# Kernel tuning notes

Measured on AMD Instinct MI355X. Metric: run time of the kernel, lower is better.

## Reference

```python
import jax, jax.numpy as jnp
import numpy as np

DIM = 256; K = 3; PAD = 1; DIL = 1; B = 16; H = 56; W = 56
SP = 8           # share_planes
RADIX = 2
ATTN = max(DIM * RADIX // 4, 32)   # 128
EMB = K * K * DIM // SP            # 288

def conv(x, w, pad=0, dil=1, groups=1):
    return jax.lax.conv_general_dilated(
        x, w, (1, 1), [(pad, pad), (pad, pad)], rhs_dilation=(dil, dil),
        feature_group_count=groups, dimension_numbers=('NCHW', 'OIHW', 'NCHW'))

def bn(x, g, b, m, v, eps=1e-5):
    # eval-mode BatchNorm2d
    s = g * jax.lax.rsqrt(v + eps)
    return x * s[None, :, None, None] + (b - m * s)[None, :, None, None]

def gn(x, g, b, groups, eps=1e-5):
    Bb, C, Hh, Ww = x.shape
    xg = x.reshape(Bb, groups, C // groups, Hh, Ww)
    mu = xg.mean((2, 3, 4), keepdims=True)
    var = xg.var((2, 3, 4), keepdims=True)
    xg = (xg - mu) * jax.lax.rsqrt(var + eps)
    return xg.reshape(Bb, C, Hh, Ww) * g[None, :, None, None] + b[None, :, None, None]

def unfold3(x):
    # im2col for 3x3, stride 1, pad 1 -> (B, C, K*K, H, W)
    Bb, C, Hh, Ww = x.shape
    p = (K - 1) // 2
    xp = jnp.pad(x, ((0, 0), (0, 0), (p, p), (p, p)))
    return jnp.stack([xp[:, :, i:i + Hh, j:j + Ww] for i in range(K) for j in range(K)], axis=2)

def reference(x, ke_w, ke_g, ke_b, ke_m, ke_v, e1_w, e1_g, e1_b, e1_m, e1_v,
              e2_w, e2_b, gng, gnb, c1_w, c1_g, c1_b, c1_m, c1_v,
              b2_g, b2_b, b2_m, b2_v, s1_w, s1_b, s1_g, s1_bb, s1_m, s1_v,
              s2_w, s2_b):
    Bb = x.shape[0]
    # key embed: grouped kxk conv + BN + ReLU
    k = jax.nn.relu(bn(conv(x, ke_w, pad=PAD, dil=DIL, groups=4), ke_g, ke_b, ke_m, ke_v))
    qk = jnp.concatenate([x, k], axis=1)                     # (B, 2*DIM, H, W)
    # dynamic kernel branch
    wemb = jax.nn.relu(bn(conv(qk, e1_w), e1_g, e1_b, e1_m, e1_v))
    wemb = conv(wemb, e2_w) + e2_b[None, :, None, None]
    wemb = gn(wemb, gng, gnb, DIM // SP)                     # GroupNorm(dim//8 groups)
    wemb = wemb.reshape(Bb, DIM // SP, K * K, H, W)
    # value branch
    xq = bn(conv(x, c1_w), c1_g, c1_b, c1_m, c1_v)
    # local dynamic convolution: per-pixel kernel shared across SP channels
    patches = unfold3(xq).reshape(Bb, DIM // SP, SP, K * K, H, W)
    y = (patches * wemb[:, :, None]).sum(3).reshape(Bb, DIM, H, W)
    y = bn(y, b2_g, b2_b, b2_m, b2_v)
    y = y * jax.nn.sigmoid(y)                                # swish
    # split attention over radix=2 branches (y, k)
    xs = jnp.stack([y, k], axis=2)                           # (B, C, 2, H, W)
    gap = xs.sum(2).mean((2, 3), keepdims=True)              # (B, C, 1, 1)
    a = jax.nn.relu(bn(conv(gap, s1_w) + s1_b[None, :, None, None], s1_g, s1_bb, s1_m, s1_v))
    a = conv(a, s2_w) + s2_b[None, :, None, None]            # (B, 2*C, 1, 1)
    a = jax.nn.softmax(a.reshape(Bb, DIM, RADIX), axis=2)
    out = (xs * a[:, :, :, None, None]).sum(2)
    return out

def setup_inputs():
    key = jax.random.key(0)
    ks = iter(jax.random.split(key, 40))
    def n(shape, s=1.0):
        return jax.random.normal(next(ks), shape, jnp.float32) * s
    def u(shape):
        return jax.random.uniform(next(ks), shape, jnp.float32, minval=0.5, maxval=1.5)
    d = {}
    d['x'] = n((B, DIM, H, W))
    d['ke_w'] = n((DIM, DIM // 4, K, K), 0.05)
    d['ke_g'] = u((DIM,)); d['ke_b'] = n((DIM,), 0.1); d['ke_m'] = n((DIM,), 0.1); d['ke_v'] = u((DIM,))
    d['e1_w'] = n((DIM // 2, 2 * DIM, 1, 1), 0.05)
    d['e1_g'] = u((DIM // 2,)); d['e1_b'] = n((DIM // 2,), 0.1); d['e1_m'] = n((DIM // 2,), 0.1); d['e1_v'] = u((DIM // 2,))
    d['e2_w'] = n((EMB, DIM // 2, 1, 1), 0.05); d['e2_b'] = n((EMB,), 0.1)
    d['gng'] = u((EMB,)); d['gnb'] = n((EMB,), 0.1)
    d['c1_w'] = n((DIM, DIM, 1, 1), 0.05)
    d['c1_g'] = u((DIM,)); d['c1_b'] = n((DIM,), 0.1); d['c1_m'] = n((DIM,), 0.1); d['c1_v'] = u((DIM,))
    d['b2_g'] = u((DIM,)); d['b2_b'] = n((DIM,), 0.1); d['b2_m'] = n((DIM,), 0.1); d['b2_v'] = u((DIM,))
    d['s1_w'] = n((ATTN, DIM, 1, 1), 0.05); d['s1_b'] = n((ATTN,), 0.1)
    d['s1_g'] = u((ATTN,)); d['s1_bb'] = n((ATTN,), 0.1); d['s1_m'] = n((ATTN,), 0.1); d['s1_v'] = u((ATTN,))
    d['s2_w'] = n((RADIX * DIM, ATTN, 1, 1), 0.05); d['s2_b'] = n((RADIX * DIM,), 0.1)
    return d
```

## Files before the change

### kernel.cpp

```cpp
#include <hip/hip_runtime.h>
#include <hip/hip_bf16.h>

typedef __hip_bfloat16 bf16;
typedef float f32x4 __attribute__((ext_vector_type(4)));
typedef short s16x8 __attribute__((ext_vector_type(8)));

#define NPIX 3136
#define HDIM 56
#define CDIM 256
#define PPIX 3364

static __device__ __forceinline__ float b2f(bf16 v){ return __bfloat162float(v); }
static __device__ __forceinline__ bf16  f2b(float v){ return __float2bfloat16(v); }

#define O_KE_S 0
#define O_KE_B 256
#define O_E1_S 512
#define O_E1_B 640
#define O_C1_S 768
#define O_C1_B 1024
#define O_B2_S 1280
#define O_B2_B 1536
#define O_S1_S 1792
#define O_S1_B 1920
#define O_E2B  2048
#define O_GNS  2336
#define O_GAP  3360
#define O_ATT  7456

__global__ void prep(
    const float* __restrict__ kew, const float* __restrict__ e1w,
    const float* __restrict__ e2w, const float* __restrict__ c1w,
    const float* keg, const float* keb, const float* kem, const float* kev,
    const float* e1g, const float* e1b, const float* e1m, const float* e1v,
    const float* e2b,
    const float* c1g, const float* c1b, const float* c1m, const float* c1v,
    const float* b2g, const float* b2b, const float* b2m, const float* b2v,
    const float* s1g, const float* s1bb, const float* s1m, const float* s1v,
    bf16* kewT, bf16* e1wb, bf16* e2wb, bf16* c1wb, float* o)
{
    int bid = blockIdx.x, t = threadIdx.x;
    if (bid < 576) {
        int i = bid * 256 + t;
        int ci = i & 63, co_l = (i >> 6) & 63;
        int gt = i >> 12;
        int tap = gt % 9, g = gt / 9;
        int co = g * 64 + co_l;
        kewT[i] = f2b(kew[(co * 64 + ci) * 9 + tap]);
    } else if (bid < 832) {
        int i = (bid - 576) * 256 + t; e1wb[i] = f2b(e1w[i]);
    } else if (bid < 976) {
        int i = (bid - 832) * 256 + t; e2wb[i] = f2b(e2w[i]);
    } else if (bid < 1232) {
        int i = (bid - 976) * 256 + t; c1wb[i] = f2b(c1w[i]);
    } else if (bid == 1232) {
        const float eps = 1e-5f;
        {
            float s = keg[t] * rsqrtf(kev[t] + eps);
            o[O_KE_S + t] = s; o[O_KE_B + t] = keb[t] - kem[t] * s;
            s = c1g[t] * rsqrtf(c1v[t] + eps);
            o[O_C1_S + t] = s; o[O_C1_B + t] = c1b[t] - c1m[t] * s;
            s = b2g[t] * rsqrtf(b2v[t] + eps);
            o[O_B2_S + t] = s; o[O_B2_B + t] = b2b[t] - b2m[t] * s;
        }
        if (t < 128) {
            float s = e1g[t] * rsqrtf(e1v[t] + eps);
            o[O_E1_S + t] = s; o[O_E1_B + t] = e1b[t] - e1m[t] * s;
            s = s1g[t] * rsqrtf(s1v[t] + eps);
            o[O_S1_S + t] = s; o[O_S1_B + t] = s1bb[t] - s1m[t] * s;
        }
        for (int i = t; i < 288; i += 256) o[O_E2B + i] = e2b[i];
    } else {
        int j = (bid - 1233) * 256 + t;
        if (j < 1024) o[O_GNS + j] = 0.f;
        else          o[O_GAP + j - 1024] = 0.f;
    }
}

__global__ __launch_bounds__(256) void cvt_x(const float* __restrict__ x, bf16* __restrict__ xh)
{
    int b = blockIdx.y;
    int p0 = blockIdx.x * 64;
    __shared__ bf16 T[64][264];
    int t = threadIdx.x;

    if (blockIdx.x == 0) {
        float4 z = {0.f, 0.f, 0.f, 0.f};
        for (int s = t; s < 7296; s += 256) {
            int pi = s >> 5, cc = s & 31;
            int pos;
            if (pi < 58)       pos = pi;
            else if (pi < 116) pos = 57 * 58 + (pi - 58);
            else if (pi < 172) pos = (pi - 115) * 58;
            else               pos = (pi - 171) * 58 + 57;
            *(float4*)(xh + ((long)b * PPIX + pos) * 256 + cc * 8) = z;
        }
    }

    for (int it = 0; it < 16; it++) {
        int slot = t + it * 256;
        int c = slot >> 4, ch4 = slot & 15;
        float4 v = *(const float4*)(x + ((long)b * CDIM + c) * NPIX + p0 + ch4 * 4);
        T[ch4 * 4 + 0][c] = f2b(v.x);
        T[ch4 * 4 + 1][c] = f2b(v.y);
        T[ch4 * 4 + 2][c] = f2b(v.z);
        T[ch4 * 4 + 3][c] = f2b(v.w);
    }
    __syncthreads();
    for (int it = 0; it < 8; it++) {
        int slot = t + it * 256;
        int p = slot >> 5, cc = slot & 31;
        int pl = p0 + p;
        int h = pl / HDIM, w = pl - h * HDIM;
        *(float4*)(xh + ((long)b * PPIX + (h + 1) * 58 + (w + 1)) * 256 + cc * 8) = *(const float4*)&T[p][cc * 8];
    }
}

__global__ __launch_bounds__(256, 4) void gconv_mfma(
    const bf16* __restrict__ xp, const bf16* __restrict__ wT,
    const float* __restrict__ scale, const float* __restrict__ bias,
    bf16* __restrict__ kh)
{
    int b = blockIdx.z, g = blockIdx.y;
    int h0 = blockIdx.x * 2;
    __shared__ bf16 As[232 * 64];
    int t = threadIdx.x;
    int wv = t >> 6, lane = t & 63, q = lane >> 4, ln = lane & 15;

    #pragma unroll
    for (int i = 0; i < 8; i++) {
        int slot = t + i * 256;
        if (slot < 1856) {
            int pos = slot >> 3, chunkL = slot & 7;
            int ri = pos / 58, ci = pos - ri * 58;
            int chunkg = chunkL ^ (pos & 7);
            float4 v = *(const float4*)(xp + (((long)b * PPIX + (h0 + ri) * 58 + ci) * 256 + g * 64 + chunkg * 8));
            *(float4*)&As[pos * 64 + chunkL * 8] = v;
        }
    }

    int posb[7];
    #pragma unroll
    for (int pt = 0; pt < 7; pt++) {
        int p = pt * 16 + ln;
        int prow = (p >= 56) ? 1 : 0;
        int pcol = p - prow * 56;
        posb[pt] = prow * 58 + pcol + 1;
    }
    const bf16* wbase = wT + ((long)(g * 9) * 64 + wv * 16 + ln) * 64;

    __syncthreads();

    f32x4 acc[7] = {};
    #pragma unroll
    for (int tap = 0; tap < 9; tap++) {
        const int dr = tap / 3;
        const int dc = tap % 3 - 1;
        const bf16* wq = wbase + tap * 64 * 64;
        s16x8 B0 = *(const s16x8*)(wq + q * 8);
        s16x8 B1 = *(const s16x8*)(wq + 32 + q * 8);
        #pragma unroll
        for (int pt = 0; pt < 7; pt++) {
            int pos = posb[pt] + dr * 58 + dc;
            int off0 = pos * 64 + ((q ^ (pos & 7)) * 8);
            s16x8 a0 = *(const s16x8*)&As[off0];
            s16x8 a1 = *(const s16x8*)&As[off0 ^ 32];
            acc[pt] = __builtin_amdgcn_mfma_f32_16x16x32_bf16(a0, B0, acc[pt], 0, 0, 0);
            acc[pt] = __builtin_amdgcn_mfma_f32_16x16x32_bf16(a1, B1, acc[pt], 0, 0, 0);
        }
    }

    __syncthreads();
    bf16* T = As;
    int co = g * 64 + wv * 16 + ln;
    float sc = scale[co], bi = bias[co];
    #pragma unroll
    for (int pt = 0; pt < 7; pt++)
        #pragma unroll
        for (int r = 0; r < 4; r++)
            T[(pt * 16 + q * 4 + r) * 72 + wv * 16 + ln] = f2b(fmaxf(acc[pt][r] * sc + bi, 0.f));
    __syncthreads();
    int pimg0 = blockIdx.x * 112;
    #pragma unroll
    for (int i = 0; i < 4; i++) {
        int slot = t + i * 256;
        if (slot < 896) {
            int row = slot >> 3, cc = slot & 7;
            *(float4*)(kh + ((long)b * NPIX + pimg0 + row) * CDIM + g * 64 + cc * 8) = *(const float4*)&T[row * 72 + cc * 8];
        }
    }
}

template<int MODE, int PADX0>
__global__ __launch_bounds__(256) void mfma_gemm(
    const bf16* __restrict__ Wt, const bf16* __restrict__ X0, const bf16* __restrict__ X1,
    int C0, int K, int M,
    const float* __restrict__ scale, const float* __restrict__ bias,
    bf16* __restrict__ Y, float* __restrict__ gnsum)
{
    int b = blockIdx.z;
    int p0 = blockIdx.x * 64;
    int m0 = blockIdx.y * 128;
    __shared__ bf16 SH[64 * 72 + 128 * 72];
    bf16* As = SH;
    bf16* Bs = SH + 64 * 72;
    __shared__ float gs[64];
    int t = threadIdx.x;
    int wv = t >> 6, lane = t & 63, q = lane >> 4, ln = lane & 15;
    if (MODE == 1) { if (t < 64) gs[t] = 0.f; }

    f32x4 acc[4][2] = {};
    for (int k0 = 0; k0 < K; k0 += 64) {
        __syncthreads();
        #pragma unroll
        for (int i = 0; i < 2; i++) {
            int slot = t + i * 256;
            int chunk = slot & 7, row = slot >> 3;
            int ch = k0 + chunk * 8;
            const bf16* src;
            if (ch < C0) {
                long pp = p0 + row;
                long pidx = PADX0 ? ((long)b * PPIX + pp + 2 * (pp / HDIM) + 59)
                                  : ((long)b * NPIX + pp);
                src = X0 + pidx * C0 + ch;
            } else {
                src = X1 + ((long)b * NPIX + p0 + row) * (K - C0) + (ch - C0);
            }
            *(float4*)&As[row * 72 + chunk * 8] = *(const float4*)src;
        }
        #pragma unroll
        for (int i = 0; i < 4; i++) {
            int slot = t + i * 256;
            int chunk = slot & 7, row = slot >> 3;
            int m = m0 + row;
            float4 v = {0.f, 0.f, 0.f, 0.f};
            if (m < M) v = *(const float4*)(Wt + (long)m * K + k0 + chunk * 8);
            *(float4*)&Bs[row * 72 + chunk * 8] = v;
        }
        __syncthreads();
        #pragma unroll
        for (int kk = 0; kk < 2; kk++) {
            s16x8 a[4];
            #pragma unroll
            for (int pt = 0; pt < 4; pt++)
                a[pt] = *(const s16x8*)&As[(pt * 16 + ln) * 72 + kk * 32 + q * 8];
            #pragma unroll
            for (int mi = 0; mi < 2; mi++) {
                s16x8 bb = *(const s16x8*)&Bs[(wv * 32 + mi * 16 + ln) * 72 + kk * 32 + q * 8];
                #pragma unroll
                for (int pt = 0; pt < 4; pt++)
                    acc[pt][mi] = __builtin_amdgcn_mfma_f32_16x16x32_bf16(a[pt], bb, acc[pt][mi], 0, 0, 0);
            }
        }
    }

    __syncthreads();
    bf16* T = SH;
    #pragma unroll
    for (int mi = 0; mi < 2; mi++) {
        int m = m0 + wv * 32 + mi * 16 + ln;
        int mc = (m > M - 1) ? (M - 1) : m;
        float sc = 1.f, bi;
        if (MODE == 0 || MODE == 2) { sc = scale[mc]; bi = bias[mc]; }
        else bi = bias[mc];
        float ps = 0.f, pq = 0.f;
        #pragma unroll
        for (int pt = 0; pt < 4; pt++) {
            #pragma unroll
            for (int r = 0; r < 4; r++) {
                float v = acc[pt][mi][r] * sc + bi;
                if (MODE == 0) v = fmaxf(v, 0.f);
                if (MODE == 1) { ps += v; pq += v * v; }
                T[(pt * 16 + q * 4 + r) * 144 + wv * 32 + mi * 16 + ln] = f2b(v);
            }
        }
        if (MODE == 1 && m < M) {
            int grp = m / 9;
            atomicAdd(&gs[grp * 2], ps);
            atomicAdd(&gs[grp * 2 + 1], pq);
        }
    }
    __syncthreads();
    #pragma unroll
    for (int i = 0; i < 4; i++) {
        int slot = t + i * 256;
        int chunk = slot & 15, row = slot >> 4;
        int m = m0 + chunk * 8;
        if (m + 8 <= M)
            *(float4*)(Y + ((long)b * NPIX + p0 + row) * M + m) = *(const float4*)&T[row * 144 + chunk * 8];
    }
    if (MODE == 1 && t < 64) atomicAdd(&gnsum[b * 64 + t], gs[t]);
}

__global__ __launch_bounds__(256) void dynconv(
    const bf16* __restrict__ xq, const bf16* __restrict__ wemb,
    const float* __restrict__ gnsum,
    const float* __restrict__ gng, const float* __restrict__ gnb,
    const float* __restrict__ b2s, const float* __restrict__ b2b,
    bf16* __restrict__ y)
{
    int id = blockIdx.x * 256 + threadIdx.x;
    int grp = id & 31;
    int p = (id >> 5) % NPIX;
    int b = id / (NPIX * 32);
    int h = p / HDIM, w = p % HDIM;
    float S = gnsum[b * 64 + grp * 2], Q = gnsum[b * 64 + grp * 2 + 1];
    float mu = S * (1.f / 28224.f);
    float var = Q * (1.f / 28224.f) - mu * mu;
    float rs = rsqrtf(fmaxf(var, 0.f) + 1e-5f);
    const bf16* wp = wemb + ((long)b * NPIX + p) * 288 + grp * 9;
    float wv[9];
    #pragma unroll
    for (int tp = 0; tp < 9; tp++)
        wv[tp] = (b2f(wp[tp]) - mu) * rs * gng[grp * 9 + tp] + gnb[grp * 9 + tp];
    float acc[8] = {};
    #pragma unroll
    for (int tp = 0; tp < 9; tp++) {
        int h2 = h + tp / 3 - 1, w2 = w + tp % 3 - 1;
        if ((unsigned)h2 >= HDIM || (unsigned)w2 >= HDIM) continue;
        const bf16* xp = xq + ((long)b * NPIX + h2 * HDIM + w2) * CDIM + grp * 8;
        s16x8 xv = *(const s16x8*)xp;
        const bf16* xb = (const bf16*)&xv;
        float wt = wv[tp];
        #pragma unroll
        for (int i = 0; i < 8; i++) acc[i] += b2f(xb[i]) * wt;
    }
    bf16 outv[8];
    #pragma unroll
    for (int i = 0; i < 8; i++) {
        int c = grp * 8 + i;
        float v = acc[i] * b2s[c] + b2b[c];
        outv[i] = f2b(v / (1.f + __expf(-v)));
    }
    *(float4*)(y + ((long)b * NPIX + p) * CDIM + grp * 8) = *(const float4*)outv;
}

__global__ __launch_bounds__(256) void gapk(const bf16* __restrict__ y, const bf16* __restrict__ k, float* __restrict__ gap)
{
    int b = blockIdx.x, chunk = blockIdx.y;
    int t = threadIdx.x;
    int cc = t & 31, pl = t >> 5;
    float acc[8] = {};
    #pragma unroll
    for (int i = 0; i < 8; i++) {
        long off = ((long)b * NPIX + chunk * 64 + pl * 8 + i) * CDIM + cc * 8;
        s16x8 yv = *(const s16x8*)(y + off);
        s16x8 kv = *(const s16x8*)(k + off);
        const bf16* ya = (const bf16*)&yv;
        const bf16* ka = (const bf16*)&kv;
        #pragma unroll
        for (int j = 0; j < 8; j++) acc[j] += b2f(ya[j]) + b2f(ka[j]);
    }
    __shared__ float R[8][256];
    #pragma unroll
    for (int j = 0; j < 8; j++) R[pl][cc * 8 + j] = acc[j];
    __syncthreads();
    float s = 0.f;
    #pragma unroll
    for (int p = 0; p < 8; p++) s += R[p][t];
    atomicAdd(&gap[b * 256 + t], s * (1.f / NPIX));
}

__global__ void attnk(const float* __restrict__ gap,
                      const float* __restrict__ s1w, const float* __restrict__ s1b,
                      const float* __restrict__ s1s, const float* __restrict__ s1bi,
                      const float* __restrict__ s2w, const float* __restrict__ s2b,
                      float* __restrict__ att)
{
    int b = blockIdx.x, t = threadIdx.x;
    __shared__ float g[256], a1[128];
    for (int i = t; i < 256; i += 128) g[i] = gap[b * 256 + i];
    __syncthreads();
    float s = 0.f;
    for (int ci = 0; ci < 256; ci++) s += s1w[t * 256 + ci] * g[ci];
    s += s1b[t];
    s = s * s1s[t] + s1bi[t];
    a1[t] = fmaxf(s, 0.f);
    __syncthreads();
    for (int c = t; c < 256; c += 128) {
        float v0 = s2b[2 * c], v1 = s2b[2 * c + 1];
        for (int ci = 0; ci < 128; ci++) {
            float av = a1[ci];
            v0 += s2w[(2 * c) * 128 + ci] * av;
            v1 += s2w[(2 * c + 1) * 128 + ci] * av;
        }
        float m = fmaxf(v0, v1);
        float e0 = __expf(v0 - m), e1 = __expf(v1 - m);
        float inv = 1.f / (e0 + e1);
        att[(b * 256 + c) * 2 + 0] = e0 * inv;
        att[(b * 256 + c) * 2 + 1] = e1 * inv;
    }
}

__global__ __launch_bounds__(256) void finalk(
    const bf16* __restrict__ y, const bf16* __restrict__ k,
    const float* __restrict__ att, float* __restrict__ out)
{
    int b = blockIdx.z, c0 = blockIdx.y * 64, p0 = blockIdx.x * 64;
    __shared__ bf16 Ys[64][72], Ks[64][72];
    int t = threadIdx.x;
    #pragma unroll
    for (int i = 0; i < 2; i++) {
        int slot = t + i * 256;
        int row = slot >> 3, cc = slot & 7;
        long off = ((long)b * NPIX + p0 + row) * CDIM + c0 + cc * 8;
        *(float4*)&Ys[row][cc * 8] = *(const float4*)(y + off);
        *(float4*)&Ks[row][cc * 8] = *(const float4*)(k + off);
    }
    __syncthreads();
    int c_l = t >> 2, pc = t & 3;
    int c = c0 + c_l;
    float a0 = att[(b * 256 + c) * 2], a1 = att[(b * 256 + c) * 2 + 1];
    float4 o[4];
    float* of = (float*)o;
    #pragma unroll
    for (int j = 0; j < 16; j++) {
        int p = pc * 16 + j;
        of[j] = b2f(Ys[p][c_l]) * a0 + b2f(Ks[p][c_l]) * a1;
    }
    float* dst = out + ((long)b * CDIM + c) * NPIX + p0 + pc * 16;
    #pragma unroll
    for (int j = 0; j < 4; j++) ((float4*)dst)[j] = o[j];
}

extern "C" void kernel_launch(void* const* d_in, const int* in_sizes, int n_in,
                              void* d_out, int out_size, void* d_ws, size_t ws_size,
                              hipStream_t stream)
{
    const float* x    = (const float*)d_in[0];
    const float* ke_w = (const float*)d_in[1];
    const float* ke_g = (const float*)d_in[2];
    const float* ke_b = (const float*)d_in[3];
    const float* ke_m = (const float*)d_in[4];
    const float* ke_v = (const float*)d_in[5];
    const float* e1_w = (const float*)d_in[6];
    const float* e1_g = (const float*)d_in[7];
    const float* e1_b = (const float*)d_in[8];
    const float* e1_m = (const float*)d_in[9];
    const float* e1_v = (const float*)d_in[10];
    const float* e2_w = (const float*)d_in[11];
    const float* e2_b = (const float*)d_in[12];
    const float* gng  = (const float*)d_in[13];
    const float* gnb  = (const float*)d_in[14];
    const float* c1_w = (const float*)d_in[15];
    const float* c1_g = (const float*)d_in[16];
    const float* c1_b = (const float*)d_in[17];
    const float* c1_m = (const float*)d_in[18];
    const float* c1_v = (const float*)d_in[19];
    const float* b2_g = (const float*)d_in[20];
    const float* b2_b = (const float*)d_in[21];
    const float* b2_m = (const float*)d_in[22];
    const float* b2_v = (const float*)d_in[23];
    const float* s1_w = (const float*)d_in[24];
    const float* s1_b = (const float*)d_in[25];
    const float* s1_g = (const float*)d_in[26];
    const float* s1_bb= (const float*)d_in[27];
    const float* s1_m = (const float*)d_in[28];
    const float* s1_v = (const float*)d_in[29];
    const float* s2_w = (const float*)d_in[30];
    const float* s2_b = (const float*)d_in[31];

    float* fold = (float*)d_ws;
    bf16* wsb   = (bf16*)((char*)d_ws + 65536);
    bf16* xh   = wsb;
    bf16* kh   = xh + 13778944L;
    bf16* wemb = kh + 12845056L;
    bf16* w1   = wemb + 14450688L;
    bf16* xq   = w1;
    bf16* yb   = xh;
    bf16* kewT = w1 + 12845056L;
    bf16* e1wb = kewT + 147456L;
    bf16* e2wb = e1wb + 65536L;
    bf16* c1wb = e2wb + 36864L;

    prep<<<dim3(1253), dim3(256), 0, stream>>>(
        ke_w, e1_w, e2_w, c1_w,
        ke_g, ke_b, ke_m, ke_v, e1_g, e1_b, e1_m, e1_v, e2_b,
        c1_g, c1_b, c1_m, c1_v, b2_g, b2_b, b2_m, b2_v,
        s1_g, s1_bb, s1_m, s1_v,
        kewT, e1wb, e2wb, c1wb, fold);

    cvt_x<<<dim3(49, 16), dim3(256), 0, stream>>>(x, xh);

    gconv_mfma<<<dim3(28, 4, 16), dim3(256), 0, stream>>>(
        xh, kewT, fold + O_KE_S, fold + O_KE_B, kh);

    mfma_gemm<0, 1><<<dim3(49, 1, 16), dim3(256), 0, stream>>>(
        e1wb, xh, kh, 256, 512, 128, fold + O_E1_S, fold + O_E1_B, w1, nullptr);

    mfma_gemm<1, 0><<<dim3(49, 3, 16), dim3(256), 0, stream>>>(
        e2wb, w1, (const bf16*)nullptr, 128, 128, 288, (const float*)nullptr, fold + O_E2B,
        wemb, fold + O_GNS);

    mfma_gemm<2, 1><<<dim3(49, 2, 16), dim3(256), 0, stream>>>(
        c1wb, xh, (const bf16*)nullptr, 256, 256, 256, fold + O_C1_S, fold + O_C1_B, xq, nullptr);

    dynconv<<<dim3(6272), dim3(256), 0, stream>>>(
        xq, wemb, fold + O_GNS, gng, gnb,
        fold + O_B2_S, fold + O_B2_B, yb);

    gapk<<<dim3(16, 49), dim3(256), 0, stream>>>(yb, kh, fold + O_GAP);

    attnk<<<dim3(16), dim3(128), 0, stream>>>(
        fold + O_GAP, s1_w, s1_b, fold + O_S1_S, fold + O_S1_B, s2_w, s2_b, fold + O_ATT);

    finalk<<<dim3(49, 4, 16), dim3(256), 0, stream>>>(yb, kh, fold + O_ATT, (float*)d_out);
}
```

Before: 352.5 us.

## Fuse global-average-pool into producers and merge e1/c1 GEMM launches

Global average pooling moves into the gconv and dynconv epilogues, where per-channel partial sums are computed from values already on chip and atomically accumulated. This removes the separate gapk kernel, which re-read both y and k from memory. The e1 and c1 1x1 GEMMs are merged into a single launch selected by blockIdx.y, so they share one grid, and the 1/NPIX scaling moves into attnk. The cost is more global atomics, and the pooled sums now use the fp32 values (and gconv's bf16 tile) rather than the re-read stored tensors, so rounding changes slightly.

```diff
diff --git a/kernel.cpp b/kernel.cpp
--- a/kernel.cpp
+++ b/kernel.cpp
@@ -119,7 +119,7 @@
 __global__ __launch_bounds__(256, 4) void gconv_mfma(
     const bf16* __restrict__ xp, const bf16* __restrict__ wT,
     const float* __restrict__ scale, const float* __restrict__ bias,
-    bf16* __restrict__ kh)
+    bf16* __restrict__ kh, float* __restrict__ gap)
 {
     int b = blockIdx.z, g = blockIdx.y;
     int h0 = blockIdx.x * 2;
@@ -189,25 +189,36 @@
             *(float4*)(kh + ((long)b * NPIX + pimg0 + row) * CDIM + g * 64 + cc * 8) = *(const float4*)&T[row * 72 + cc * 8];
         }
     }
-}
-
-template<int MODE, int PADX0>
-__global__ __launch_bounds__(256) void mfma_gemm(
-    const bf16* __restrict__ Wt, const bf16* __restrict__ X0, const bf16* __restrict__ X1,
-    int C0, int K, int M,
-    const float* __restrict__ scale, const float* __restrict__ bias,
-    bf16* __restrict__ Y, float* __restrict__ gnsum)
+    {
+        int co_l = t & 63, rb = t >> 6;
+        float s = 0.f;
+        #pragma unroll
+        for (int r = 0; r < 28; r++) s += b2f(T[(rb * 28 + r) * 72 + co_l]);
+        atomicAdd(&gap[b * 256 + g * 64 + co_l], s);
+    }
+}
+
+__global__ __launch_bounds__(256) void gemm_pair(
+    const bf16* __restrict__ e1w, const bf16* __restrict__ c1w,
+    const bf16* __restrict__ X0, const bf16* __restrict__ X1,
+    const float* __restrict__ fold,
+    bf16* __restrict__ Ye1, bf16* __restrict__ Yc1)
 {
     int b = blockIdx.z;
     int p0 = blockIdx.x * 64;
-    int m0 = blockIdx.y * 128;
+    int by = blockIdx.y;
+    const bf16* Wt; int K, M, m0; const float *scp, *bip; bf16* Y; bool relu;
+    if (by == 0) { Wt = e1w; K = 512; M = 128; m0 = 0;
+                   scp = fold + O_E1_S; bip = fold + O_E1_B; Y = Ye1; relu = true; }
+    else         { Wt = c1w; K = 256; M = 256; m0 = (by - 1) * 128;
+                   scp = fold + O_C1_S; bip = fold + O_C1_B; Y = Yc1; relu = false; }
+    const int C0 = 256;
+
     __shared__ bf16 SH[64 * 72 + 128 * 72];
     bf16* As = SH;
     bf16* Bs = SH + 64 * 72;
-    __shared__ float gs[64];
     int t = threadIdx.x;
     int wv = t >> 6, lane = t & 63, q = lane >> 4, ln = lane & 15;
-    if (MODE == 1) { if (t < 64) gs[t] = 0.f; }
 
     f32x4 acc[4][2] = {};
     for (int k0 = 0; k0 < K; k0 += 64) {
@@ -220,11 +231,10 @@
             const bf16* src;
             if (ch < C0) {
                 long pp = p0 + row;
-                long pidx = PADX0 ? ((long)b * PPIX + pp + 2 * (pp / HDIM) + 59)
-                                  : ((long)b * NPIX + pp);
+                long pidx = (long)b * PPIX + pp + 2 * (pp / HDIM) + 59;
                 src = X0 + pidx * C0 + ch;
             } else {
-                src = X1 + ((long)b * NPIX + p0 + row) * (K - C0) + (ch - C0);
+                src = X1 + ((long)b * NPIX + p0 + row) * 256 + (ch - C0);
             }
             *(float4*)&As[row * 72 + chunk * 8] = *(const float4*)src;
         }
@@ -232,10 +242,7 @@
         for (int i = 0; i < 4; i++) {
             int slot = t + i * 256;
             int chunk = slot & 7, row = slot >> 3;
-            int m = m0 + row;
-            float4 v = {0.f, 0.f, 0.f, 0.f};
-            if (m < M) v = *(const float4*)(Wt + (long)m * K + k0 + chunk * 8);
-            *(float4*)&Bs[row * 72 + chunk * 8] = v;
+            *(float4*)&Bs[row * 72 + chunk * 8] = *(const float4*)(Wt + (long)(m0 + row) * K + k0 + chunk * 8);
         }
         __syncthreads();
         #pragma unroll
@@ -259,22 +266,107 @@
     #pragma unroll
     for (int mi = 0; mi < 2; mi++) {
         int m = m0 + wv * 32 + mi * 16 + ln;
-        int mc = (m > M - 1) ? (M - 1) : m;
-        float sc = 1.f, bi;
-        if (MODE == 0 || MODE == 2) { sc = scale[mc]; bi = bias[mc]; }
-        else bi = bias[mc];
-        float ps = 0.f, pq = 0.f;
+        float sc = scp[m], bi = bip[m];
         #pragma unroll
         for (int pt = 0; pt < 4; pt++) {
             #pragma unroll
             for (int r = 0; r < 4; r++) {
                 float v = acc[pt][mi][r] * sc + bi;
-                if (MODE == 0) v = fmaxf(v, 0.f);
-                if (MODE == 1) { ps += v; pq += v * v; }
+                if (relu) v = fmaxf(v, 0.f);
                 T[(pt * 16 + q * 4 + r) * 144 + wv * 32 + mi * 16 + ln] = f2b(v);
             }
         }
-        if (MODE == 1 && m < M) {
+    }
+    __syncthreads();
+    int nst = (M == 128) ? 2 : 4;
+    for (int i = 0; i < nst; i++) {
+        int slot = t + i * 256;
+        int chunk = slot & (2 * (M / 128) * 8 - 1), row = slot / (2 * (M / 128) * 8);
+        ;
+    }
+    {
+        int chunks = M / 8;
+        int total = 64 * chunks;
+        for (int slot = t; slot < total; slot += 256) {
+            int row = slot / chunks, chunk = slot - row * chunks;
+            int m = m0 + chunk * 8;
+            if (m < m0 + 128)
+                *(float4*)(Y + ((long)b * NPIX + p0 + row) * M + m) = *(const float4*)&T[row * 144 + chunk * 8];
+        }
+    }
+}
+
+__global__ __launch_bounds__(256) void mfma_gemm_e2(
+    const bf16* __restrict__ Wt, const bf16* __restrict__ X0,
+    const float* __restrict__ bias,
+    bf16* __restrict__ Y, float* __restrict__ gnsum)
+{
+    const int K = 128, M = 288;
+    int b = blockIdx.z;
+    int p0 = blockIdx.x * 64;
+    int m0 = blockIdx.y * 128;
+    __shared__ bf16 SH[64 * 72 + 128 * 72];
+    bf16* As = SH;
+    bf16* Bs = SH + 64 * 72;
+    __shared__ float gs[64];
+    int t = threadIdx.x;
+    int wv = t >> 6, lane = t & 63, q = lane >> 4, ln = lane & 15;
+    if (t < 64) gs[t] = 0.f;
+
+    f32x4 acc[4][2] = {};
+    for (int k0 = 0; k0 < K; k0 += 64) {
+        __syncthreads();
+        #pragma unroll
+        for (int i = 0; i < 2; i++) {
+            int slot = t + i * 256;
+            int chunk = slot & 7, row = slot >> 3;
+            int ch = k0 + chunk * 8;
+            *(float4*)&As[row * 72 + chunk * 8] = *(const float4*)(X0 + ((long)b * NPIX + p0 + row) * K + ch);
+        }
+        #pragma unroll
+        for (int i = 0; i < 4; i++) {
+            int slot = t + i * 256;
+            int chunk = slot & 7, row = slot >> 3;
+            int m = m0 + row;
+            float4 v = {0.f, 0.f, 0.f, 0.f};
+            if (m < M) v = *(const float4*)(Wt + (long)m * K + k0 + chunk * 8);
+            *(float4*)&Bs[row * 72 + chunk * 8] = v;
+        }
+        __syncthreads();
+        #pragma unroll
+        for (int kk = 0; kk < 2; kk++) {
+            s16x8 a[4];
+            #pragma unroll
+            for (int pt = 0; pt < 4; pt++)
+                a[pt] = *(const s16x8*)&As[(pt * 16 + ln) * 72 + kk * 32 + q * 8];
+            #pragma unroll
+            for (int mi = 0; mi < 2; mi++) {
+                s16x8 bb = *(const s16x8*)&Bs[(wv * 32 + mi * 16 + ln) * 72 + kk * 32 + q * 8];
+                #pragma unroll
+                for (int pt = 0; pt < 4; pt++)
+                    acc[pt][mi] = __builtin_amdgcn_mfma_f32_16x16x32_bf16(a[pt], bb, acc[pt][mi], 0, 0, 0);
+            }
+        }
+    }
+
+    __syncthreads();
+    bf16* T = SH;
+    #pragma unroll
+    for (int mi = 0; mi < 2; mi++) {
+        int m = m0 + wv * 32 + mi * 16 + ln;
+        int mc = (m > M - 1) ? (M - 1) : m;
+        float bi = bias[mc];
+        float ps = 0.f, pq = 0.f;
+        #pragma unroll
+        for (int pt = 0; pt < 4; pt++) {
+            #pragma unroll
+            for (int r = 0; r < 4; r++) {
+                float v = acc[pt][mi][r] + bi;
+                ps += v; pq += v * v;
+                T[(pt * 16 + q * 4 + r) * 144 + wv * 32 + mi * 16 + ln] = f2b(v);
+            }
+        }
+        if (m < M) {
             int grp = m / 9;
             atomicAdd(&gs[grp * 2], ps);
             atomicAdd(&gs[grp * 2 + 1], pq);
@@ -289,7 +381,7 @@
         if (m + 8 <= M)
             *(float4*)(Y + ((long)b * NPIX + p0 + row) * M + m) = *(const float4*)&T[row * 144 + chunk * 8];
     }
-    if (MODE == 1 && t < 64) atomicAdd(&gnsum[b * 64 + t], gs[t]);
+    if (t < 64) atomicAdd(&gnsum[b * 64 + t], gs[t]);
 }
 
 __global__ __launch_bounds__(256) void dynconv(
@@ -297,7 +389,7 @@
     const float* __restrict__ gnsum,
     const float* __restrict__ gng, const float* __restrict__ gnb,
     const float* __restrict__ b2s, const float* __restrict__ b2b,
-    bf16* __restrict__ y)
+    bf16* __restrict__ y, float* __restrict__ gap)
 {
     int id = blockIdx.x * 256 + threadIdx.x;
     int grp = id & 31;
@@ -326,39 +418,26 @@
         for (int i = 0; i < 8; i++) acc[i] += b2f(xb[i]) * wt;
     }
     bf16 outv[8];
+    float sv[8];
     #pragma unroll
     for (int i = 0; i < 8; i++) {
         int c = grp * 8 + i;
         float v = acc[i] * b2s[c] + b2b[c];
-        outv[i] = f2b(v / (1.f + __expf(-v)));
+        float sw = v / (1.f + __expf(-v));
+        sv[i] = sw;
+        outv[i] = f2b(sw);
     }
     *(float4*)(y + ((long)b * NPIX + p) * CDIM + grp * 8) = *(const float4*)outv;
-}
-
-__global__ __launch_bounds__(256) void gapk(const bf16* __restrict__ y, const bf16* __restrict__ k, float* __restrict__ gap)
-{
-    int b = blockIdx.x, chunk = blockIdx.y;
-    int t = threadIdx.x;
-    int cc = t & 31, pl = t >> 5;
-    float acc[8] = {};
-    #pragma unroll
-    for (int i = 0; i < 8; i++) {
-        long off = ((long)b * NPIX + chunk * 64 + pl * 8 + i) * CDIM + cc * 8;
-        s16x8 yv = *(const s16x8*)(y + off);
-        s16x8 kv = *(const s16x8*)(k + off);
-        const bf16* ya = (const bf16*)&yv;
-        const bf16* ka = (const bf16*)&kv;
-        #pragma unroll
-        for (int j = 0; j < 8; j++) acc[j] += b2f(ya[j]) + b2f(ka[j]);
-    }
+
     __shared__ float R[8][256];
-    #pragma unroll
-    for (int j = 0; j < 8; j++) R[pl][cc * 8 + j] = acc[j];
+    int pl = threadIdx.x >> 5;
+    #pragma unroll
+    for (int i = 0; i < 8; i++) R[pl][grp * 8 + i] = sv[i];
     __syncthreads();
     float s = 0.f;
     #pragma unroll
-    for (int p = 0; p < 8; p++) s += R[p][t];
-    atomicAdd(&gap[b * 256 + t], s * (1.f / NPIX));
+    for (int j = 0; j < 8; j++) s += R[j][threadIdx.x];
+    atomicAdd(&gap[b * 256 + threadIdx.x], s);
 }
 
 __global__ void attnk(const float* __restrict__ gap,
@@ -369,7 +448,7 @@
 {
     int b = blockIdx.x, t = threadIdx.x;
     __shared__ float g[256], a1[128];
-    for (int i = t; i < 256; i += 128) g[i] = gap[b * 256 + i];
+    for (int i = t; i < 256; i += 128) g[i] = gap[b * 256 + i] * (1.f / NPIX);
     __syncthreads();
     float s = 0.f;
     for (int ci = 0; ci < 256; ci++) s += s1w[t * 256 + ci] * g[ci];
@@ -466,12 +545,12 @@
     bf16* kh   = xh + 13778944L;
     bf16* wemb = kh + 12845056L;
     bf16* w1   = wemb + 14450688L;
-    bf16* xq   = w1;
-    bf16* yb   = xh;
-    bf16* kewT = w1 + 12845056L;
+    bf16* kewT = w1 + 6422528L;
     bf16* e1wb = kewT + 147456L;
     bf16* e2wb = e1wb + 65536L;
     bf16* c1wb = e2wb + 36864L;
+    bf16* xq   = c1wb + 65536L;
+    bf16* yb   = xh;
 
     prep<<<dim3(1253), dim3(256), 0, stream>>>(
         ke_w, e1_w, e2_w, c1_w,
@@ -483,23 +562,17 @@
     cvt_x<<<dim3(49, 16), dim3(256), 0, stream>>>(x, xh);
 
     gconv_mfma<<<dim3(28, 4, 16), dim3(256), 0, stream>>>(
-        xh, kewT, fold + O_KE_S, fold + O_KE_B, kh);
-
-    mfma_gemm<0, 1><<<dim3(49, 1, 16), dim3(256), 0, stream>>>(
-        e1wb, xh, kh, 256, 512, 128, fold + O_E1_S, fold + O_E1_B, w1, nullptr);
-
-    mfma_gemm<1, 0><<<dim3(49, 3, 16), dim3(256), 0, stream>>>(
-        e2wb, w1, (const bf16*)nullptr, 128, 128, 288, (const float*)nullptr, fold + O_E2B,
-        wemb, fold + O_GNS);
-
-    mfma_gemm<2, 1><<<dim3(49, 2, 16), dim3(256), 0, stream>>>(
-        c1wb, xh, (const bf16*)nullptr, 256, 256, 256, fold + O_C1_S, fold + O_C1_B, xq, nullptr);
+        xh, kewT, fold + O_KE_S, fold + O_KE_B, kh, fold + O_GAP);
+
+    gemm_pair<<<dim3(49, 3, 16), dim3(256), 0, stream>>>(
+        e1wb, c1wb, xh, kh, fold, w1, xq);
+
+    mfma_gemm_e2<<<dim3(49, 3, 16), dim3(256), 0, stream>>>(
+        e2wb, w1, fold + O_E2B, wemb, fold + O_GNS);
 
     dynconv<<<dim3(6272), dim3(256), 0, stream>>>(
         xq, wemb, fold + O_GNS, gng, gnb,
-        fold + O_B2_S, fold + O_B2_B, yb);
-
-    gapk<<<dim3(16, 49), dim3(256), 0, stream>>>(yb, kh, fold + O_GAP);
+        fold + O_B2_S, fold + O_B2_B, yb, fold + O_GAP);
 
     attnk<<<dim3(16), dim3(128), 0, stream>>>(
         fold + O_GAP, s1_w, s1_b, fold + O_S1_S, fold + O_S1_B, s2_w, s2_b, fold + O_ATT);
```

Result: no change. 351.2 us (-0.4%).
